# Performance work log

Hardware: AMD Instinct MI355X
Metric: run time of the kernel (lower is better)

Reference implementation:

```python
import jax, jax.numpy as jnp
import numpy as np

D_MODEL = 1024
N_HEADS = 16
N_KV = 4
HD = D_MODEL // N_HEADS  # 64
N_REP = N_HEADS // N_KV
WINDOW = 128
SCALE = HD ** -0.5
B, T = 2, 2048


def _rope(x):
    # x: [B, H, T, hd]; half-split rotate_half RoPE, base 10000
    t = x.shape[2]
    hd = x.shape[-1]
    inv_freq = 1.0 / (10000.0 ** (jnp.arange(0, hd, 2, dtype=jnp.float32) / hd))
    freqs = jnp.arange(t, dtype=jnp.float32)[:, None] * inv_freq[None, :]  # [T, hd/2]
    cos = jnp.cos(freqs)[None, None]  # [1,1,T,hd/2]
    sin = jnp.sin(freqs)[None, None]
    x1, x2 = x[..., : hd // 2], x[..., hd // 2:]
    return jnp.concatenate([x1 * cos - x2 * sin, x1 * sin + x2 * cos], axis=-1)


def setup_inputs() -> dict:
    key = jax.random.key(0)
    ks = jax.random.split(key, 6)
    s = 0.02
    return {
        "query": jax.random.normal(ks[0], (B, T, D_MODEL), dtype=jnp.float32),
        "Wq": jax.random.normal(ks[1], (D_MODEL, D_MODEL), dtype=jnp.float32) * s,
        "Wk": jax.random.normal(ks[2], (N_KV * HD, D_MODEL), dtype=jnp.float32) * s,
        "Wv": jax.random.normal(ks[3], (N_KV * HD, D_MODEL), dtype=jnp.float32) * s,
        "W1": jax.random.normal(ks[4], (4 * D_MODEL, D_MODEL), dtype=jnp.float32) * s,
        "W2": jax.random.normal(ks[5], (D_MODEL, 4 * D_MODEL), dtype=jnp.float32) * s,
    }


def reference(query, Wq, Wk, Wv, W1, W2):
    b, t, _ = query.shape
    # QKV projections (nn.Linear, no bias): x @ W.T
    q = (query @ Wq.T).reshape(b, t, N_HEADS, HD).transpose(0, 2, 1, 3)  # [B,H,T,hd]
    k = (query @ Wk.T).reshape(b, t, N_KV, HD).transpose(0, 2, 1, 3)    # [B,Hkv,T,hd]
    v = (query @ Wv.T).reshape(b, t, N_KV, HD).transpose(0, 2, 1, 3)
    # Rotary embeddings on q/k (self-attention)
    q = _rope(q)
    k = _rope(k)
    # GQA: repeat kv heads (kv-head-major ordering, matches torch expand+reshape)
    k = jnp.repeat(k, N_REP, axis=1)
    v = jnp.repeat(v, N_REP, axis=1)
    # scores + causal sliding-window band mask (True = masked)
    scores = jnp.einsum("bhqd,bhkd->bhqk", q, k) * SCALE
    i = jnp.arange(t)[:, None]
    j = jnp.arange(t)[None, :]
    mask = (j > i) | (j < i - (WINDOW - 1))  # causal window of size WINDOW
    scores = jnp.where(mask[None, None], jnp.float32(-1e30), scores)
    attn = jax.nn.softmax(scores, axis=-1)
    out = jnp.einsum("bhqk,bhkd->bhqd", attn, v)
    out = out.transpose(0, 2, 1, 3).reshape(b, t, D_MODEL)
    # out_proj: Linear(d,4d) -> SiLU -> Linear(4d,d)
    h = out @ W1.T
    h = h * jax.nn.sigmoid(h)
    return h @ W2.T
```

## Files before the change

### kernel.cpp

```cpp
#include <hip/hip_runtime.h>
#include <math.h>


typedef __bf16 bf16x8 __attribute__((ext_vector_type(8)));
typedef __bf16 bf16x4 __attribute__((ext_vector_type(4)));
typedef float  f32x4  __attribute__((ext_vector_type(4)));

extern __shared__ __align__(16) char smem[];

#define GLOAD_LDS16(g, l) __builtin_amdgcn_global_load_lds(               \
    (const __attribute__((address_space(1))) void*)(g),                   \
    (__attribute__((address_space(3))) void*)(l), 16, 0, 0)

__device__ __forceinline__ unsigned pk2(float a, float b) {
    union { __bf16 h[2]; unsigned u; } t;
    t.h[0] = (__bf16)a; t.h[1] = (__bf16)b;
    return t.u;
}

__device__ __forceinline__ int xcd_swz(int bid, int n) {
    return (bid & 7) * (n >> 3) + (bid >> 3);
}

__global__ __launch_bounds__(256) void MultiAttention_60722247631706_conv(
    const float* x, const float* Wq, const float* Wk, const float* Wv,
    const float* W1, const float* W2, float* out, float* ws, int phase)
{
    __bf16* xbf    = (__bf16*)(ws + 6291456);
    __bf16* wqkvbf = (__bf16*)(ws + 8388608);
    __bf16* w1bf   = (__bf16*)(ws + 10485760);
    __bf16* w2bf   = (__bf16*)(ws + 8388608);
    const int tid = threadIdx.x;

    if (phase == 5) {
        const long long total4 = 9961472 / 4;
        for (long long i4 = (long long)blockIdx.x * 256 + tid; i4 < total4;
             i4 += (long long)gridDim.x * 256) {
            const long long i = i4 * 4;
            const float* src; __bf16* dst;
            if (i < 4194304)      { src = x  + i;             dst = xbf    + i; }
            else if (i < 5242880) { src = Wq + (i - 4194304); dst = wqkvbf + (i - 4194304); }
            else if (i < 5505024) { src = Wk + (i - 5242880); dst = wqkvbf + (i - 4194304); }
            else if (i < 5767168) { src = Wv + (i - 5505024); dst = wqkvbf + (i - 4194304); }
            else                  { src = W1 + (i - 5767168); dst = w1bf   + (i - 5767168); }
            const f32x4 v = *(const f32x4*)src;
            bf16x4 o;
            o[0] = (__bf16)v[0]; o[1] = (__bf16)v[1];
            o[2] = (__bf16)v[2]; o[3] = (__bf16)v[3];
            *(bf16x4*)dst = o;
        }
    } else {
        const long long total4 = 4194304 / 4;
        for (long long i4 = (long long)blockIdx.x * 256 + tid; i4 < total4;
             i4 += (long long)gridDim.x * 256) {
            const long long i = i4 * 4;
            const f32x4 v = *(const f32x4*)(W2 + i);
            bf16x4 o;
            o[0] = (__bf16)v[0]; o[1] = (__bf16)v[1];
            o[2] = (__bf16)v[2]; o[3] = (__bf16)v[3];
            *(bf16x4*)(w2bf + i) = o;
        }
        const f32x4 z = {0.f, 0.f, 0.f, 0.f};
        for (long long i4 = (long long)blockIdx.x * 256 + tid; i4 < total4;
             i4 += (long long)gridDim.x * 256) {
            *(f32x4*)(out + i4 * 4) = z;
        }
    }
}

__global__ __launch_bounds__(256) void MultiAttention_60722247631706_attn(
    float* ws)
{
    const float* Y = ws;
    __bf16* obf = (__bf16*)(ws + 8388608);

    __bf16* Ks = (__bf16*)smem;
    __bf16* Vt = Ks + 192 * 72;

    const int sb  = xcd_swz(blockIdx.x, 256);
    const int qt  = sb & 31;
    const int kvh = (sb >> 5) & 3;
    const int b   = sb >> 7;
    const int q0  = qt * 64;
    const int wb  = q0 - 128;

    const int tid  = threadIdx.x;
    const int w    = tid >> 6;
    const int lane = tid & 63;
    const int l16  = lane & 15;
    const int quad = lane >> 4;
    const int h    = kvh * 4 + w;

    const float* Yb = Y + (size_t)b * 2048 * 1536;

    for (int i = tid; i < 192 * 8; i += 256) {
        const int r  = i >> 3;
        const int c8 = (i & 7) * 8;
        const int j  = wb + r;
        bf16x8 kv;
        if (j >= 0) {
            const float* kp = Yb + (size_t)j * 1536 + 1024 + kvh * 64 + c8;
            const f32x4 a = *(const f32x4*)kp;
            const f32x4 c = *(const f32x4*)(kp + 4);
            kv[0] = (__bf16)a[0]; kv[1] = (__bf16)a[1];
            kv[2] = (__bf16)a[2]; kv[3] = (__bf16)a[3];
            kv[4] = (__bf16)c[0]; kv[5] = (__bf16)c[1];
            kv[6] = (__bf16)c[2]; kv[7] = (__bf16)c[3];
        } else {
            const __bf16 z = (__bf16)0.f;
            kv[0]=z; kv[1]=z; kv[2]=z; kv[3]=z; kv[4]=z; kv[5]=z; kv[6]=z; kv[7]=z;
        }
        *(bf16x8*)(Ks + r * 72 + c8) = kv;
    }
    for (int i = tid; i < 192 * 16; i += 256) {
        const int r  = i >> 4;
        const int c4 = (i & 15) * 4;
        const int j  = wb + r;
        f32x4 vv = {0.f, 0.f, 0.f, 0.f};
        if (j >= 0) vv = *(const f32x4*)(Yb + (size_t)j * 1536 + 1280 + kvh * 64 + c4);
        Vt[(c4 + 0) * 200 + r] = (__bf16)vv[0];
        Vt[(c4 + 1) * 200 + r] = (__bf16)vv[1];
        Vt[(c4 + 2) * 200 + r] = (__bf16)vv[2];
        Vt[(c4 + 3) * 200 + r] = (__bf16)vv[3];
    }

    bf16x8 qf[4][2];
#pragma unroll
    for (int qn = 0; qn < 4; ++qn)
#pragma unroll
        for (int kk = 0; kk < 2; ++kk) {
            const float* qp = Yb + (size_t)(q0 + qn * 16 + l16) * 1536
                              + h * 64 + kk * 32 + quad * 8;
            const f32x4 a = *(const f32x4*)qp;
            const f32x4 c = *(const f32x4*)(qp + 4);
            bf16x8 t;
            t[0] = (__bf16)(a[0] * 0.125f); t[1] = (__bf16)(a[1] * 0.125f);
            t[2] = (__bf16)(a[2] * 0.125f); t[3] = (__bf16)(a[3] * 0.125f);
            t[4] = (__bf16)(c[0] * 0.125f); t[5] = (__bf16)(c[1] * 0.125f);
            t[6] = (__bf16)(c[2] * 0.125f); t[7] = (__bf16)(c[3] * 0.125f);
            qf[qn][kk] = t;
        }

    __syncthreads();

    f32x4 oacc[4][4];
#pragma unroll
    for (int qm = 0; qm < 4; ++qm)
#pragma unroll
        for (int dn = 0; dn < 4; ++dn) {
            f32x4 z = {0.f, 0.f, 0.f, 0.f};
            oacc[qm][dn] = z;
        }
    float m_run[4] = {-1e30f, -1e30f, -1e30f, -1e30f};
    float l_run[4] = {0.f, 0.f, 0.f, 0.f};

    const int kclip = -wb;

    for (int kb = 0; kb < 3; ++kb) {
        f32x4 s[4][4];
#pragma unroll
        for (int km = 0; km < 4; ++km)
#pragma unroll
            for (int qn = 0; qn < 4; ++qn) {
                f32x4 z = {0.f, 0.f, 0.f, 0.f};
                s[km][qn] = z;
            }
#pragma unroll
        for (int kk = 0; kk < 2; ++kk) {
            bf16x8 kf[4];
#pragma unroll
            for (int km = 0; km < 4; ++km)
                kf[km] = *(const bf16x8*)(Ks + (kb * 64 + km * 16 + l16) * 72
                                          + kk * 32 + quad * 8);
#pragma unroll
            for (int km = 0; km < 4; ++km)
#pragma unroll
                for (int qn = 0; qn < 4; ++qn)
                    s[km][qn] = __builtin_amdgcn_mfma_f32_16x16x32_bf16(
                        kf[km], qf[qn][kk], s[km][qn], 0, 0, 0);
        }

        unsigned cu[4][4][2];
        float corr[4];
#pragma unroll
        for (int qn = 0; qn < 4; ++qn) {
            float mx = -1e30f;
#pragma unroll
            for (int km = 0; km < 4; ++km)
#pragma unroll
                for (int r = 0; r < 4; ++r) {
                    const int kl  = kb * 64 + km * 16 + quad * 4 + r;
                    const int dlt = kl - (qn * 16 + l16);
                    const bool ok = (dlt >= 1) && (dlt <= 128) && (kl >= kclip);
                    const float sv = ok ? s[km][qn][r] : -1e30f;
                    s[km][qn][r] = sv;
                    mx = fmaxf(mx, sv);
                }
            mx = fmaxf(mx, __shfl_xor(mx, 16));
            mx = fmaxf(mx, __shfl_xor(mx, 32));
            const float mnew = fmaxf(fmaxf(m_run[qn], mx), -1e20f);
            corr[qn] = expf(m_run[qn] - mnew);
            m_run[qn] = mnew;
            float rowsum = 0.f;
#pragma unroll
            for (int km = 0; km < 4; ++km) {
#pragma unroll
                for (int r = 0; r < 4; ++r) {
                    const float p = expf(s[km][qn][r] - mnew);
                    s[km][qn][r] = p;
                    rowsum += p;
                }
                cu[qn][km][0] = pk2(s[km][qn][0], s[km][qn][1]);
                cu[qn][km][1] = pk2(s[km][qn][2], s[km][qn][3]);
            }
            rowsum += __shfl_xor(rowsum, 16);
            rowsum += __shfl_xor(rowsum, 32);
            l_run[qn] = l_run[qn] * corr[qn] + rowsum;
        }

#pragma unroll
        for (int qm = 0; qm < 4; ++qm)
#pragma unroll
            for (int r = 0; r < 4; ++r) {
                const float f = __shfl(corr[qm], (lane & 48) | (quad * 4 + r));
                oacc[qm][0][r] *= f; oacc[qm][1][r] *= f;
                oacc[qm][2][r] *= f; oacc[qm][3][r] *= f;
            }

#pragma unroll
        for (int kk = 0; kk < 2; ++kk) {
            bf16x8 vf[4];
#pragma unroll
            for (int dn = 0; dn < 4; ++dn)
                vf[dn] = *(const bf16x8*)(Vt + (dn * 16 + l16) * 200
                                          + kb * 64 + kk * 32 + quad * 8);
            const int srcA = ((quad & 1) * 32) + l16;
            const int hi   = quad >> 1;
#pragma unroll
            for (int qm = 0; qm < 4; ++qm) {
                const unsigned a0 = (unsigned)__shfl((int)cu[qm][2*kk  ][0], srcA);
                const unsigned a1 = (unsigned)__shfl((int)cu[qm][2*kk  ][1], srcA);
                const unsigned b0 = (unsigned)__shfl((int)cu[qm][2*kk+1][0], srcA);
                const unsigned b1 = (unsigned)__shfl((int)cu[qm][2*kk+1][1], srcA);
                const unsigned c0 = (unsigned)__shfl((int)cu[qm][2*kk  ][0], srcA + 16);
                const unsigned c1 = (unsigned)__shfl((int)cu[qm][2*kk  ][1], srcA + 16);
                const unsigned d0 = (unsigned)__shfl((int)cu[qm][2*kk+1][0], srcA + 16);
                const unsigned d1 = (unsigned)__shfl((int)cu[qm][2*kk+1][1], srcA + 16);
                union { unsigned u[4]; bf16x8 v; } af;
                af.u[0] = hi ? b0 : a0;
                af.u[1] = hi ? b1 : a1;
                af.u[2] = hi ? d0 : c0;
                af.u[3] = hi ? d1 : c1;
#pragma unroll
                for (int dn = 0; dn < 4; ++dn)
                    oacc[qm][dn] = __builtin_amdgcn_mfma_f32_16x16x32_bf16(
                        af.v, vf[dn], oacc[qm][dn], 0, 0, 0);
            }
        }
    }

#pragma unroll
    for (int qm = 0; qm < 4; ++qm) {
        const float rl = 1.f / l_run[qm];
#pragma unroll
        for (int r = 0; r < 4; ++r) {
            const float f = __shfl(rl, (lane & 48) | (quad * 4 + r));
            const int q = q0 + qm * 16 + quad * 4 + r;
            __bf16* op = obf + ((size_t)(b * 2048 + q)) * 1024 + h * 64 + l16;
#pragma unroll
            for (int dn = 0; dn < 4; ++dn)
                op[dn * 16] = (__bf16)(oacc[qm][dn][r] * f);
        }
    }
}

__global__ __launch_bounds__(256, 4) void MultiAttention_60722247631706_p0(
    float* ws)
{
    float*  Y      = ws;
    __bf16* xbf    = (__bf16*)(ws + 6291456);
    __bf16* wqkvbf = (__bf16*)(ws + 8388608);

    const int tid = threadIdx.x;

    __bf16* As = (__bf16*)smem;
    __bf16* Bs = As + 64 * 64;

    const int bid  = xcd_swz(blockIdx.x, 768);
    const int tm   = bid / 12;
    const int tn   = bid % 12;
    const int w    = tid >> 6;
    const int lane = tid & 63;
    const int wr   = w >> 1;
    const int wc   = w & 1;
    const int l16  = lane & 15;
    const int quad = lane >> 4;
    const int srow = lane >> 3;
    const int sch  = ((lane & 7) ^ srow) * 8;

    const __bf16* ga0 = xbf    + (size_t)(tm * 64  + w * 16 + srow) * 1024 + sch;
    const __bf16* gb0 = wqkvbf + (size_t)(tn * 128 + w * 32 + srow) * 1024 + sch;

    f32x4 zero = {0.f, 0.f, 0.f, 0.f};
    f32x4 acc[2][4];
#pragma unroll
    for (int mi = 0; mi < 2; ++mi)
#pragma unroll
        for (int ni = 0; ni < 4; ++ni) acc[mi][ni] = zero;

    for (int k0 = 0; k0 < 1024; k0 += 64) {
#pragma unroll
        for (int i = 0; i < 2; ++i)
            GLOAD_LDS16(ga0 + (size_t)i * 8 * 1024 + k0, As + (w * 16 + i * 8) * 64);
#pragma unroll
        for (int i = 0; i < 4; ++i)
            GLOAD_LDS16(gb0 + (size_t)i * 8 * 1024 + k0, Bs + (w * 32 + i * 8) * 64);
        __syncthreads();
#pragma unroll
        for (int kk = 0; kk < 2; ++kk) {
            const int cs = ((kk * 4 + quad) ^ (l16 & 7)) * 8;
            bf16x8 af[2], bfr[4];
#pragma unroll
            for (int mi = 0; mi < 2; ++mi)
                af[mi] = *(const bf16x8*)(As + (size_t)(wr * 32 + mi * 16 + l16) * 64 + cs);
#pragma unroll
            for (int ni = 0; ni < 4; ++ni)
                bfr[ni] = *(const bf16x8*)(Bs + (size_t)(wc * 64 + ni * 16 + l16) * 64 + cs);
#pragma unroll
            for (int mi = 0; mi < 2; ++mi)
#pragma unroll
                for (int ni = 0; ni < 4; ++ni)
                    acc[mi][ni] = __builtin_amdgcn_mfma_f32_16x16x32_bf16(
                        af[mi], bfr[ni], acc[mi][ni], 0, 0, 0);
        }
        __syncthreads();
    }

    const int mbase = tm * 64 + wr * 32;
    const int nbase = tn * 128 + wc * 64;

    const bool rot = nbase < 1280;
    const float inv1 = powf(10000.f, -(float)l16 / 32.f);
    const float inv2 = powf(10000.f, -(float)(16 + l16) / 32.f);
#pragma unroll
    for (int mi = 0; mi < 2; ++mi) {
#pragma unroll
        for (int r = 0; r < 4; ++r) {
            const int m = mbase + mi * 16 + quad * 4 + r;
            const int t = m & 2047;
            float v0 = acc[mi][0][r], v1 = acc[mi][1][r];
            float v2 = acc[mi][2][r], v3 = acc[mi][3][r];
            if (rot) {
                const float a1 = (float)t * inv1, a2 = (float)t * inv2;
                const float c1 = cosf(a1), s1 = sinf(a1);
                const float c2 = cosf(a2), s2 = sinf(a2);
                const float n0 = v0 * c1 - v2 * s1;
                const float n2 = v0 * s1 + v2 * c1;
                const float n1 = v1 * c2 - v3 * s2;
                const float n3 = v1 * s2 + v3 * c2;
                v0 = n0; v1 = n1; v2 = n2; v3 = n3;
            }
            float* yp = Y + (size_t)m * 1536 + nbase + l16;
            yp[0] = v0; yp[16] = v1; yp[32] = v2; yp[48] = v3;
        }
    }
}

__global__ __launch_bounds__(256, 4) void MultiAttention_60722247631706_ffn1(
    float* ws)
{
    __bf16* obf  = (__bf16*)(ws + 8388608);
    __bf16* w1bf = (__bf16*)(ws + 10485760);
    __bf16* hbf  = (__bf16*)ws;

    const int tid = threadIdx.x;

    __bf16* As = (__bf16*)smem;
    __bf16* Bs = As + 128 * 64;

    const int bid  = xcd_swz(blockIdx.x, 1024);
    const int tm   = bid >> 5;
    const int tn   = bid & 31;
    const int w    = tid >> 6;
    const int lane = tid & 63;
    const int wr   = w >> 1;
    const int wc   = w & 1;
    const int l16  = lane & 15;
    const int quad = lane >> 4;
    const int srow = lane >> 3;
    const int sch  = ((lane & 7) ^ srow) * 8;

    const __bf16* ga0 = obf  + (size_t)(tm * 128 + w * 32 + srow) * 1024 + sch;
    const __bf16* gb0 = w1bf + (size_t)(tn * 128 + w * 32 + srow) * 1024 + sch;

    f32x4 zero = {0.f, 0.f, 0.f, 0.f};
    f32x4 acc[4][4];
#pragma unroll
    for (int mi = 0; mi < 4; ++mi)
#pragma unroll
        for (int ni = 0; ni < 4; ++ni) acc[mi][ni] = zero;

    for (int k0 = 0; k0 < 1024; k0 += 64) {
#pragma unroll
        for (int i = 0; i < 4; ++i) {
            GLOAD_LDS16(ga0 + (size_t)i * 8 * 1024 + k0, As + (w * 32 + i * 8) * 64);
            GLOAD_LDS16(gb0 + (size_t)i * 8 * 1024 + k0, Bs + (w * 32 + i * 8) * 64);
        }
        __syncthreads();
#pragma unroll
        for (int kk = 0; kk < 2; ++kk) {
            const int cs = ((kk * 4 + quad) ^ (l16 & 7)) * 8;
            bf16x8 af[4], bfr[4];
#pragma unroll
            for (int mi = 0; mi < 4; ++mi)
                af[mi] = *(const bf16x8*)(As + (size_t)(wr * 64 + mi * 16 + l16) * 64 + cs);
#pragma unroll
            for (int ni = 0; ni < 4; ++ni)
                bfr[ni] = *(const bf16x8*)(Bs + (size_t)(wc * 64 + ni * 16 + l16) * 64 + cs);
#pragma unroll
            for (int mi = 0; mi < 4; ++mi)
#pragma unroll
                for (int ni = 0; ni < 4; ++ni)
                    acc[mi][ni] = __builtin_amdgcn_mfma_f32_16x16x32_bf16(
                        af[mi], bfr[ni], acc[mi][ni], 0, 0, 0);
        }
        __syncthreads();
    }

#pragma unroll
    for (int mi = 0; mi < 4; ++mi) {
#pragma unroll
        for (int r = 0; r < 4; ++r) {
            const int m = tm * 128 + wr * 64 + mi * 16 + quad * 4 + r;
            __bf16* hp = hbf + (size_t)m * 4096 + tn * 128 + wc * 64 + l16;
#pragma unroll
            for (int ni = 0; ni < 4; ++ni) {
                const float v = acc[mi][ni][r];
                hp[ni * 16] = (__bf16)(v / (1.f + expf(-v)));
            }
        }
    }
}

__global__ __launch_bounds__(256, 4) void MultiAttention_60722247631706_ffn2(
    float* out, float* ws)
{
    __bf16* hbf  = (__bf16*)ws;
    __bf16* w2bf = (__bf16*)(ws + 8388608);

    int bid = xcd_swz(blockIdx.x, 1024);
    const int ks = bid >> 9;  bid &= 511;
    const int tm = bid >> 3;
    const int tn = bid & 7;
    const int kbase = ks * 2048;

    const int tid  = threadIdx.x;
    const int w    = tid >> 6;
    const int lane = tid & 63;
    const int wr   = w >> 1;
    const int wc   = w & 1;
    const int l16  = lane & 15;
    const int quad = lane >> 4;
    const int srow = lane >> 3;
    const int sch  = ((lane & 7) ^ srow) * 8;

    __bf16* As = (__bf16*)smem;
    __bf16* Bs = As + 64 * 64;

    const __bf16* ga0 = hbf  + (size_t)(tm * 64  + w * 16 + srow) * 4096 + kbase + sch;
    const __bf16* gb0 = w2bf + (size_t)(tn * 128 + w * 32 + srow) * 4096 + kbase + sch;

    f32x4 zero = {0.f, 0.f, 0.f, 0.f};
    f32x4 acc[2][4];
#pragma unroll
    for (int mi = 0; mi < 2; ++mi)
#pragma unroll
        for (int ni = 0; ni < 4; ++ni) acc[mi][ni] = zero;

    for (int k0 = 0; k0 < 2048; k0 += 64) {
#pragma unroll
        for (int i = 0; i < 2; ++i)
            GLOAD_LDS16(ga0 + (size_t)i * 8 * 4096 + k0, As + (w * 16 + i * 8) * 64);
#pragma unroll
        for (int i = 0; i < 4; ++i)
            GLOAD_LDS16(gb0 + (size_t)i * 8 * 4096 + k0, Bs + (w * 32 + i * 8) * 64);
        __syncthreads();
#pragma unroll
        for (int kk = 0; kk < 2; ++kk) {
            const int cs = ((kk * 4 + quad) ^ (l16 & 7)) * 8;
            bf16x8 af[2], bfr[4];
#pragma unroll
            for (int mi = 0; mi < 2; ++mi)
                af[mi] = *(const bf16x8*)(As + (size_t)(wr * 32 + mi * 16 + l16) * 64 + cs);
#pragma unroll
            for (int ni = 0; ni < 4; ++ni)
                bfr[ni] = *(const bf16x8*)(Bs + (size_t)(wc * 64 + ni * 16 + l16) * 64 + cs);
#pragma unroll
            for (int mi = 0; mi < 2; ++mi)
#pragma unroll
                for (int ni = 0; ni < 4; ++ni)
                    acc[mi][ni] = __builtin_amdgcn_mfma_f32_16x16x32_bf16(
                        af[mi], bfr[ni], acc[mi][ni], 0, 0, 0);
        }
        __syncthreads();
    }

#pragma unroll
    for (int mi = 0; mi < 2; ++mi) {
#pragma unroll
        for (int r = 0; r < 4; ++r) {
            const int m = tm * 64 + wr * 32 + mi * 16 + quad * 4 + r;
            float* op = out + (size_t)m * 1024 + tn * 128 + wc * 64 + l16;
#pragma unroll
            for (int ni = 0; ni < 4; ++ni)
                atomicAdd(op + ni * 16, acc[mi][ni][r]);
        }
    }
}

extern "C" void kernel_launch(void* const* d_in, const int* in_sizes, int n_in,
                              void* d_out, int out_size, void* d_ws, size_t ws_size,
                              hipStream_t stream)
{
    const float* x  = (const float*)d_in[0];
    const float* Wq = (const float*)d_in[1];
    const float* Wk = (const float*)d_in[2];
    const float* Wv = (const float*)d_in[3];
    const float* W1 = (const float*)d_in[4];
    const float* W2 = (const float*)d_in[5];
    float* out = (float*)d_out;
    float* ws  = (float*)d_ws;

    const int P0_LDS   = (64 + 128) * 64 * 2;
    const int ATTN_LDS = (192 * 72 + 64 * 200) * 2;
    const int FFN1_LDS = 2 * 128 * 64 * 2;
    const int FFN2_LDS = (64 + 128) * 64 * 2;

    MultiAttention_60722247631706_conv<<<2048, 256, 0, stream>>>(
        x, Wq, Wk, Wv, W1, W2, out, ws, 5);
    MultiAttention_60722247631706_p0<<<768, 256, P0_LDS, stream>>>(ws);
    MultiAttention_60722247631706_attn<<<256, 256, ATTN_LDS, stream>>>(ws);
    MultiAttention_60722247631706_ffn1<<<1024, 256, FFN1_LDS, stream>>>(ws);
    MultiAttention_60722247631706_conv<<<1024, 256, 0, stream>>>(
        x, Wq, Wk, Wv, W1, W2, out, ws, 6);
    MultiAttention_60722247631706_ffn2<<<1024, 256, FFN2_LDS, stream>>>(out, ws);
}
```

Measured before the change: 249.5 us.

## Emit bf16 Q/K/transposed-V from projection; shrink attention tiles and drop LDS staging

The QKV projection epilogue now writes pre-scaled bf16 Q, bf16 K and a transposed bf16 V layout, replacing the fp32 Y buffer. The attention kernel no longer stages K/V through LDS. It reads fragments straight from global memory and handles 16 queries per block instead of 64, launching four times as many blocks. This cuts the fp32 traffic and the conversion and transpose work inside attention, and raises occupancy. In exchange, K/V reuse across query tiles now depends on the L2 cache rather than shared memory.

```diff
diff --git a/kernel.cpp b/kernel.cpp
--- a/kernel.cpp
+++ b/kernel.cpp
@@ -68,20 +68,19 @@
     }
 }
 
-__global__ __launch_bounds__(256) void MultiAttention_60722247631706_attn(
+__global__ __launch_bounds__(256, 4) void MultiAttention_60722247631706_attn(
     float* ws)
 {
-    const float* Y = ws;
-    __bf16* obf = (__bf16*)(ws + 8388608);
-
-    __bf16* Ks = (__bf16*)smem;
-    __bf16* Vt = Ks + 192 * 72;
-
-    const int sb  = xcd_swz(blockIdx.x, 256);
-    const int qt  = sb & 31;
-    const int kvh = (sb >> 5) & 3;
-    const int b   = sb >> 7;
-    const int q0  = qt * 64;
+    const __bf16* qbf  = (const __bf16*)ws;
+    const __bf16* kbf  = (const __bf16*)(ws + 2097152);
+    const __bf16* vtbf = (const __bf16*)(ws + 2621440);
+    __bf16*       obf  = (__bf16*)(ws + 8388608);
+
+    const int sb  = xcd_swz(blockIdx.x, 1024);
+    const int qt  = sb & 127;
+    const int kvh = (sb >> 7) & 3;
+    const int b   = sb >> 9;
+    const int q0  = qt * 16;
     const int wb  = q0 - 128;
 
     const int tid  = threadIdx.x;
@@ -91,193 +90,137 @@
     const int quad = lane >> 4;
     const int h    = kvh * 4 + w;
 
-    const float* Yb = Y + (size_t)b * 2048 * 1536;
-
-    for (int i = tid; i < 192 * 8; i += 256) {
-        const int r  = i >> 3;
-        const int c8 = (i & 7) * 8;
-        const int j  = wb + r;
-        bf16x8 kv;
-        if (j >= 0) {
-            const float* kp = Yb + (size_t)j * 1536 + 1024 + kvh * 64 + c8;
-            const f32x4 a = *(const f32x4*)kp;
-            const f32x4 c = *(const f32x4*)(kp + 4);
-            kv[0] = (__bf16)a[0]; kv[1] = (__bf16)a[1];
-            kv[2] = (__bf16)a[2]; kv[3] = (__bf16)a[3];
-            kv[4] = (__bf16)c[0]; kv[5] = (__bf16)c[1];
-            kv[6] = (__bf16)c[2]; kv[7] = (__bf16)c[3];
-        } else {
-            const __bf16 z = (__bf16)0.f;
-            kv[0]=z; kv[1]=z; kv[2]=z; kv[3]=z; kv[4]=z; kv[5]=z; kv[6]=z; kv[7]=z;
-        }
-        *(bf16x8*)(Ks + r * 72 + c8) = kv;
-    }
-    for (int i = tid; i < 192 * 16; i += 256) {
-        const int r  = i >> 4;
-        const int c4 = (i & 15) * 4;
-        const int j  = wb + r;
-        f32x4 vv = {0.f, 0.f, 0.f, 0.f};
-        if (j >= 0) vv = *(const f32x4*)(Yb + (size_t)j * 1536 + 1280 + kvh * 64 + c4);
-        Vt[(c4 + 0) * 200 + r] = (__bf16)vv[0];
-        Vt[(c4 + 1) * 200 + r] = (__bf16)vv[1];
-        Vt[(c4 + 2) * 200 + r] = (__bf16)vv[2];
-        Vt[(c4 + 3) * 200 + r] = (__bf16)vv[3];
-    }
-
-    bf16x8 qf[4][2];
-#pragma unroll
-    for (int qn = 0; qn < 4; ++qn)
-#pragma unroll
-        for (int kk = 0; kk < 2; ++kk) {
-            const float* qp = Yb + (size_t)(q0 + qn * 16 + l16) * 1536
-                              + h * 64 + kk * 32 + quad * 8;
-            const f32x4 a = *(const f32x4*)qp;
-            const f32x4 c = *(const f32x4*)(qp + 4);
-            bf16x8 t;
-            t[0] = (__bf16)(a[0] * 0.125f); t[1] = (__bf16)(a[1] * 0.125f);
-            t[2] = (__bf16)(a[2] * 0.125f); t[3] = (__bf16)(a[3] * 0.125f);
-            t[4] = (__bf16)(c[0] * 0.125f); t[5] = (__bf16)(c[1] * 0.125f);
-            t[6] = (__bf16)(c[2] * 0.125f); t[7] = (__bf16)(c[3] * 0.125f);
-            qf[qn][kk] = t;
-        }
-
-    __syncthreads();
-
-    f32x4 oacc[4][4];
-#pragma unroll
-    for (int qm = 0; qm < 4; ++qm)
-#pragma unroll
-        for (int dn = 0; dn < 4; ++dn) {
+    const __bf16* Kb = kbf + (size_t)b * 2048 * 256 + kvh * 64;
+    const __bf16* Vb = vtbf + (size_t)(b * 4 + kvh) * 64 * 2048;
+
+    bf16x8 qf[2];
+#pragma unroll
+    for (int kk = 0; kk < 2; ++kk)
+        qf[kk] = *(const bf16x8*)(qbf + (size_t)(b * 2048 + q0 + l16) * 1024
+                                  + h * 64 + kk * 32 + quad * 8);
+
+    f32x4 oacc[4];
+#pragma unroll
+    for (int dn = 0; dn < 4; ++dn) {
+        f32x4 z = {0.f, 0.f, 0.f, 0.f};
+        oacc[dn] = z;
+    }
+    float m_run = -1e30f, l_run = 0.f;
+    const int kclip = -wb;
+
+    for (int kb = 0; kb < 3; ++kb) {
+        f32x4 s[4];
+#pragma unroll
+        for (int km = 0; km < 4; ++km) {
             f32x4 z = {0.f, 0.f, 0.f, 0.f};
-            oacc[qm][dn] = z;
-        }
-    float m_run[4] = {-1e30f, -1e30f, -1e30f, -1e30f};
-    float l_run[4] = {0.f, 0.f, 0.f, 0.f};
-
-    const int kclip = -wb;
-
-    for (int kb = 0; kb < 3; ++kb) {
-        f32x4 s[4][4];
-#pragma unroll
-        for (int km = 0; km < 4; ++km)
-#pragma unroll
-            for (int qn = 0; qn < 4; ++qn) {
-                f32x4 z = {0.f, 0.f, 0.f, 0.f};
-                s[km][qn] = z;
-            }
+            s[km] = z;
+        }
 #pragma unroll
         for (int kk = 0; kk < 2; ++kk) {
             bf16x8 kf[4];
 #pragma unroll
+            for (int km = 0; km < 4; ++km) {
+                int row = wb + kb * 64 + km * 16 + l16;
+                row = (row >= 0 && row < 2048) ? row : 0;
+                kf[km] = *(const bf16x8*)(Kb + (size_t)row * 256
+                                          + kk * 32 + quad * 8);
+            }
+#pragma unroll
             for (int km = 0; km < 4; ++km)
-                kf[km] = *(const bf16x8*)(Ks + (kb * 64 + km * 16 + l16) * 72
-                                          + kk * 32 + quad * 8);
-#pragma unroll
-            for (int km = 0; km < 4; ++km)
-#pragma unroll
-                for (int qn = 0; qn < 4; ++qn)
-                    s[km][qn] = __builtin_amdgcn_mfma_f32_16x16x32_bf16(
-                        kf[km], qf[qn][kk], s[km][qn], 0, 0, 0);
-        }
-
-        unsigned cu[4][4][2];
-        float corr[4];
-#pragma unroll
-        for (int qn = 0; qn < 4; ++qn) {
-            float mx = -1e30f;
-#pragma unroll
-            for (int km = 0; km < 4; ++km)
-#pragma unroll
-                for (int r = 0; r < 4; ++r) {
-                    const int kl  = kb * 64 + km * 16 + quad * 4 + r;
-                    const int dlt = kl - (qn * 16 + l16);
-                    const bool ok = (dlt >= 1) && (dlt <= 128) && (kl >= kclip);
-                    const float sv = ok ? s[km][qn][r] : -1e30f;
-                    s[km][qn][r] = sv;
-                    mx = fmaxf(mx, sv);
-                }
-            mx = fmaxf(mx, __shfl_xor(mx, 16));
-            mx = fmaxf(mx, __shfl_xor(mx, 32));
-            const float mnew = fmaxf(fmaxf(m_run[qn], mx), -1e20f);
-            corr[qn] = expf(m_run[qn] - mnew);
-            m_run[qn] = mnew;
-            float rowsum = 0.f;
-#pragma unroll
-            for (int km = 0; km < 4; ++km) {
-#pragma unroll
-                for (int r = 0; r < 4; ++r) {
-                    const float p = expf(s[km][qn][r] - mnew);
-                    s[km][qn][r] = p;
-                    rowsum += p;
-                }
-                cu[qn][km][0] = pk2(s[km][qn][0], s[km][qn][1]);
-                cu[qn][km][1] = pk2(s[km][qn][2], s[km][qn][3]);
-            }
-            rowsum += __shfl_xor(rowsum, 16);
-            rowsum += __shfl_xor(rowsum, 32);
-            l_run[qn] = l_run[qn] * corr[qn] + rowsum;
-        }
-
-#pragma unroll
-        for (int qm = 0; qm < 4; ++qm)
+                s[km] = __builtin_amdgcn_mfma_f32_16x16x32_bf16(
+                    kf[km], qf[kk], s[km], 0, 0, 0);
+        }
+
+        float mx = -1e30f;
+#pragma unroll
+        for (int km = 0; km < 4; ++km)
 #pragma unroll
             for (int r = 0; r < 4; ++r) {
-                const float f = __shfl(corr[qm], (lane & 48) | (quad * 4 + r));
-                oacc[qm][0][r] *= f; oacc[qm][1][r] *= f;
-                oacc[qm][2][r] *= f; oacc[qm][3][r] *= f;
-            }
+                const int kl  = kb * 64 + km * 16 + quad * 4 + r;
+                const int dlt = kl - l16;
+                const bool ok = (dlt >= 1) && (dlt <= 128) && (kl >= kclip);
+                const float sv = ok ? s[km][r] : -1e30f;
+                s[km][r] = sv;
+                mx = fmaxf(mx, sv);
+            }
+        mx = fmaxf(mx, __shfl_xor(mx, 16));
+        mx = fmaxf(mx, __shfl_xor(mx, 32));
+        const float mnew = fmaxf(fmaxf(m_run, mx), -1e20f);
+        const float corr = expf(m_run - mnew);
+        m_run = mnew;
+        float rowsum = 0.f;
+        unsigned cu[4][2];
+#pragma unroll
+        for (int km = 0; km < 4; ++km) {
+#pragma unroll
+            for (int r = 0; r < 4; ++r) {
+                const float p = expf(s[km][r] - mnew);
+                s[km][r] = p;
+                rowsum += p;
+            }
+            cu[km][0] = pk2(s[km][0], s[km][1]);
+            cu[km][1] = pk2(s[km][2], s[km][3]);
+        }
+        rowsum += __shfl_xor(rowsum, 16);
+        rowsum += __shfl_xor(rowsum, 32);
+        l_run = l_run * corr + rowsum;
+
+#pragma unroll
+        for (int r = 0; r < 4; ++r) {
+            const float f = __shfl(corr, (lane & 48) | (quad * 4 + r));
+            oacc[0][r] *= f; oacc[1][r] *= f;
+            oacc[2][r] *= f; oacc[3][r] *= f;
+        }
 
 #pragma unroll
         for (int kk = 0; kk < 2; ++kk) {
             bf16x8 vf[4];
 #pragma unroll
-            for (int dn = 0; dn < 4; ++dn)
-                vf[dn] = *(const bf16x8*)(Vt + (dn * 16 + l16) * 200
-                                          + kb * 64 + kk * 32 + quad * 8);
+            for (int dn = 0; dn < 4; ++dn) {
+                int t = wb + kb * 64 + kk * 32 + quad * 8;
+                t = (t >= 0 && t <= 2040) ? t : 0;
+                vf[dn] = *(const bf16x8*)(Vb + (size_t)(dn * 16 + l16) * 2048 + t);
+            }
             const int srcA = ((quad & 1) * 32) + l16;
             const int hi   = quad >> 1;
-#pragma unroll
-            for (int qm = 0; qm < 4; ++qm) {
-                const unsigned a0 = (unsigned)__shfl((int)cu[qm][2*kk  ][0], srcA);
-                const unsigned a1 = (unsigned)__shfl((int)cu[qm][2*kk  ][1], srcA);
-                const unsigned b0 = (unsigned)__shfl((int)cu[qm][2*kk+1][0], srcA);
-                const unsigned b1 = (unsigned)__shfl((int)cu[qm][2*kk+1][1], srcA);
-                const unsigned c0 = (unsigned)__shfl((int)cu[qm][2*kk  ][0], srcA + 16);
-                const unsigned c1 = (unsigned)__shfl((int)cu[qm][2*kk  ][1], srcA + 16);
-                const unsigned d0 = (unsigned)__shfl((int)cu[qm][2*kk+1][0], srcA + 16);
-                const unsigned d1 = (unsigned)__shfl((int)cu[qm][2*kk+1][1], srcA + 16);
-                union { unsigned u[4]; bf16x8 v; } af;
-                af.u[0] = hi ? b0 : a0;
-                af.u[1] = hi ? b1 : a1;
-                af.u[2] = hi ? d0 : c0;
-                af.u[3] = hi ? d1 : c1;
-#pragma unroll
-                for (int dn = 0; dn < 4; ++dn)
-                    oacc[qm][dn] = __builtin_amdgcn_mfma_f32_16x16x32_bf16(
-                        af.v, vf[dn], oacc[qm][dn], 0, 0, 0);
-            }
-        }
-    }
-
-#pragma unroll
-    for (int qm = 0; qm < 4; ++qm) {
-        const float rl = 1.f / l_run[qm];
-#pragma unroll
-        for (int r = 0; r < 4; ++r) {
-            const float f = __shfl(rl, (lane & 48) | (quad * 4 + r));
-            const int q = q0 + qm * 16 + quad * 4 + r;
-            __bf16* op = obf + ((size_t)(b * 2048 + q)) * 1024 + h * 64 + l16;
+            const unsigned a0 = (unsigned)__shfl((int)cu[2*kk  ][0], srcA);
+            const unsigned a1 = (unsigned)__shfl((int)cu[2*kk  ][1], srcA);
+            const unsigned b0 = (unsigned)__shfl((int)cu[2*kk+1][0], srcA);
+            const unsigned b1 = (unsigned)__shfl((int)cu[2*kk+1][1], srcA);
+            const unsigned c0 = (unsigned)__shfl((int)cu[2*kk  ][0], srcA + 16);
+            const unsigned c1 = (unsigned)__shfl((int)cu[2*kk  ][1], srcA + 16);
+            const unsigned d0 = (unsigned)__shfl((int)cu[2*kk+1][0], srcA + 16);
+            const unsigned d1 = (unsigned)__shfl((int)cu[2*kk+1][1], srcA + 16);
+            union { unsigned u[4]; bf16x8 v; } af;
+            af.u[0] = hi ? b0 : a0;
+            af.u[1] = hi ? b1 : a1;
+            af.u[2] = hi ? d0 : c0;
+            af.u[3] = hi ? d1 : c1;
 #pragma unroll
             for (int dn = 0; dn < 4; ++dn)
-                op[dn * 16] = (__bf16)(oacc[qm][dn][r] * f);
-        }
+                oacc[dn] = __builtin_amdgcn_mfma_f32_16x16x32_bf16(
+                    af.v, vf[dn], oacc[dn], 0, 0, 0);
+        }
+    }
+
+    const float rl = 1.f / l_run;
+#pragma unroll
+    for (int r = 0; r < 4; ++r) {
+        const float f = __shfl(rl, (lane & 48) | (quad * 4 + r));
+        const int q = q0 + quad * 4 + r;
+        __bf16* op = obf + ((size_t)(b * 2048 + q)) * 1024 + h * 64 + l16;
+#pragma unroll
+        for (int dn = 0; dn < 4; ++dn)
+            op[dn * 16] = (__bf16)(oacc[dn][r] * f);
     }
 }
 
 __global__ __launch_bounds__(256, 4) void MultiAttention_60722247631706_p0(
     float* ws)
 {
-    float*  Y      = ws;
+    __bf16* qbf    = (__bf16*)ws;
+    __bf16* kbf    = (__bf16*)(ws + 2097152);
+    __bf16* vtbf   = (__bf16*)(ws + 2621440);
     __bf16* xbf    = (__bf16*)(ws + 6291456);
     __bf16* wqkvbf = (__bf16*)(ws + 8388608);
 
@@ -339,29 +282,48 @@
     const int mbase = tm * 64 + wr * 32;
     const int nbase = tn * 128 + wc * 64;
 
-    const bool rot = nbase < 1280;
-    const float inv1 = powf(10000.f, -(float)l16 / 32.f);
-    const float inv2 = powf(10000.f, -(float)(16 + l16) / 32.f);
-#pragma unroll
-    for (int mi = 0; mi < 2; ++mi) {
-#pragma unroll
-        for (int r = 0; r < 4; ++r) {
-            const int m = mbase + mi * 16 + quad * 4 + r;
-            const int t = m & 2047;
-            float v0 = acc[mi][0][r], v1 = acc[mi][1][r];
-            float v2 = acc[mi][2][r], v3 = acc[mi][3][r];
-            if (rot) {
+    if (nbase < 1280) {
+        const bool isQ = nbase < 1024;
+        const float inv1 = powf(10000.f, -(float)l16 / 32.f);
+        const float inv2 = powf(10000.f, -(float)(16 + l16) / 32.f);
+#pragma unroll
+        for (int mi = 0; mi < 2; ++mi) {
+#pragma unroll
+            for (int r = 0; r < 4; ++r) {
+                const int m = mbase + mi * 16 + quad * 4 + r;
+                const int t = m & 2047;
+                float v0 = acc[mi][0][r], v1 = acc[mi][1][r];
+                float v2 = acc[mi][2][r], v3 = acc[mi][3][r];
                 const float a1 = (float)t * inv1, a2 = (float)t * inv2;
                 const float c1 = cosf(a1), s1 = sinf(a1);
                 const float c2 = cosf(a2), s2 = sinf(a2);
-                const float n0 = v0 * c1 - v2 * s1;
-                const float n2 = v0 * s1 + v2 * c1;
-                const float n1 = v1 * c2 - v3 * s2;
-                const float n3 = v1 * s2 + v3 * c2;
-                v0 = n0; v1 = n1; v2 = n2; v3 = n3;
-            }
-            float* yp = Y + (size_t)m * 1536 + nbase + l16;
-            yp[0] = v0; yp[16] = v1; yp[32] = v2; yp[48] = v3;
+                float n0 = v0 * c1 - v2 * s1;
+                float n2 = v0 * s1 + v2 * c1;
+                float n1 = v1 * c2 - v3 * s2;
+                float n3 = v1 * s2 + v3 * c2;
+                if (isQ) { n0 *= 0.125f; n1 *= 0.125f; n2 *= 0.125f; n3 *= 0.125f; }
+                __bf16* dst = isQ
+                    ? qbf + (size_t)m * 1024 + nbase + l16
+                    : kbf + (size_t)m * 256 + (nbase - 1024) + l16;
+                dst[0]  = (__bf16)n0; dst[16] = (__bf16)n1;
+                dst[32] = (__bf16)n2; dst[48] = (__bf16)n3;
+            }
+        }
+    } else {
+        const int kvh = (nbase - 1280) >> 6;
+        const int bb  = mbase >> 11;
+        const int tb  = mbase & 2047;
+#pragma unroll
+        for (int mi = 0; mi < 2; ++mi) {
+#pragma unroll
+            for (int ni = 0; ni < 4; ++ni) {
+                const int d = ni * 16 + l16;
+                bf16x4 pv;
+                pv[0] = (__bf16)acc[mi][ni][0]; pv[1] = (__bf16)acc[mi][ni][1];
+                pv[2] = (__bf16)acc[mi][ni][2]; pv[3] = (__bf16)acc[mi][ni][3];
+                *(bf16x4*)(vtbf + ((size_t)(bb * 4 + kvh) * 64 + d) * 2048
+                           + tb + mi * 16 + quad * 4) = pv;
+            }
         }
     }
 }
@@ -532,14 +494,13 @@
     float* ws  = (float*)d_ws;
 
     const int P0_LDS   = (64 + 128) * 64 * 2;
-    const int ATTN_LDS = (192 * 72 + 64 * 200) * 2;
     const int FFN1_LDS = 2 * 128 * 64 * 2;
     const int FFN2_LDS = (64 + 128) * 64 * 2;
 
     MultiAttention_60722247631706_conv<<<2048, 256, 0, stream>>>(
         x, Wq, Wk, Wv, W1, W2, out, ws, 5);
     MultiAttention_60722247631706_p0<<<768, 256, P0_LDS, stream>>>(ws);
-    MultiAttention_60722247631706_attn<<<256, 256, ATTN_LDS, stream>>>(ws);
+    MultiAttention_60722247631706_attn<<<1024, 256, 0, stream>>>(ws);
     MultiAttention_60722247631706_ffn1<<<1024, 256, FFN1_LDS, stream>>>(ws);
     MultiAttention_60722247631706_conv<<<1024, 256, 0, stream>>>(
         x, Wq, Wk, Wv, W1, W2, out, ws, 6);
```

Result: no change. 247.0 us (-1.0%).
